# Kernel optimization log

Measured on AMD Instinct MI355X. Metric: run time of the kernel, lower is better.

## Reference

```python
import jax, jax.numpy as jnp
import numpy as np
from math import sqrt

B, LT, LM = 4, 512, 1024
HID, NH, HD = 512, 8, 64          # self-attn: hidden, n_head, head_size
NHP, KS = 16, 64                  # cross-attn: 2*max_charge*n_head_per_mass, key_size
FF = 4 * HID
ALPHA = 2.0
EPS = 1e-5


def apply_rope(x, dis):
    # dis: same trailing dim as x; chunk into (sin, cos) halves
    s, c = jnp.split(dis, 2, axis=-1)
    x0, x1 = x[..., 0::2], x[..., 1::2]
    return jnp.concatenate([x0 * c - x1 * s, x1 * c + x0 * s], axis=-1)


def layer_norm(x, g, b):
    mu = jnp.mean(x, axis=-1, keepdims=True)
    var = jnp.mean(jnp.square(x - mu), axis=-1, keepdims=True)
    return (x - mu) * jax.lax.rsqrt(var + EPS) * g + b


def deep_norm(x, postx, g, b):
    # dropout is identity in eval mode
    return layer_norm(x * ALPHA + postx, g, b)


def attn_block(x_q, x_kv, dis_q, dis_k, wq, bq, wk, bk, wv, bv, wo, bo, mask, n_head, head_size):
    bsz = x_q.shape[0]
    q = (x_q @ wq.T + bq).reshape(bsz, -1, n_head, head_size)
    k = (x_kv @ wk.T + bk).reshape(bsz, -1, n_head, head_size)
    v = (x_kv @ wv.T + bv).reshape(bsz, -1, n_head, head_size)
    q = apply_rope(q, dis_q)
    k = apply_rope(k, dis_k)
    attn = jnp.einsum('bnhd,bmhd->bhnm', q, k) / sqrt(head_size)  # [B,H,Lq,Lk]
    attn = jnp.where(mask, attn, -jnp.inf)
    attn = jax.nn.softmax(attn, axis=-1)
    out = jnp.einsum('bhnm,bmhd->bnhd', attn, v).reshape(bsz, -1, n_head * head_size)
    return out @ wo.T + bo


def setup_inputs() -> dict:
    key = jax.random.key(0)
    ks = jax.random.split(key, 32)
    rn = lambda i, shape, s=1.0: jax.random.normal(ks[i], shape, jnp.float32) * s
    inp = {}
    inp['tgt'] = rn(0, (B, LT, HID))
    inp['mem'] = rn(1, (B, LM, HID))
    inp['glycan_mass'] = rn(2, (B, LT, NH, HD))
    inp['glycan_query_mass'] = rn(3, (B, LT, NH, HD))
    inp['glycan_crossattn_mass'] = rn(4, (B, LT, NHP, KS))
    inp['node_mass_emb'] = rn(5, (B, LM, NHP, KS))
    inp['node_mass'] = rn(6, (B, LM))
    causal = jnp.tril(jnp.ones((LT, LT), bool))
    inp['tgt_mask'] = jnp.broadcast_to(causal[None, None], (B, 1, LT, LT))
    inp['rel_mask'] = jnp.ones((B, 1, LT, LM), bool)
    inp['layer'] = 0
    inp['A'] = rn(7, (1,))
    w = 0.03  # param init scale
    # self-attn params
    inp['wq1'] = rn(8, (HID, HID), w);  inp['bq1'] = jnp.zeros((HID,))
    inp['wk1'] = rn(9, (HID, HID), w);  inp['bk1'] = jnp.zeros((HID,))
    inp['wv1'] = rn(10, (HID, HID), w); inp['bv1'] = jnp.zeros((HID,))
    inp['wo1'] = rn(11, (HID, HID), w); inp['bo1'] = jnp.zeros((HID,))
    inp['ln1_g'] = jnp.ones((HID,));    inp['ln1_b'] = jnp.zeros((HID,))
    # cross-attn params (projection dim NHP*KS = 1024)
    P = NHP * KS
    inp['wq2'] = rn(12, (P, HID), w);   inp['bq2'] = jnp.zeros((P,))
    inp['wk2'] = rn(13, (P, HID), w);   inp['bk2'] = jnp.zeros((P,))
    inp['wv2'] = rn(14, (P, HID), w);   inp['bv2'] = jnp.zeros((P,))
    inp['wo2'] = rn(15, (HID, P), w);   inp['bo2'] = jnp.zeros((HID,))
    inp['ln2_g'] = jnp.ones((HID,));    inp['ln2_b'] = jnp.zeros((HID,))
    # FFN params (no bias) + DeepNorm LN
    inp['w_ff1'] = rn(16, (FF, HID), w)
    inp['w_ff2'] = rn(17, (HID, FF), w)
    inp['ln3_g'] = jnp.ones((HID,));    inp['ln3_b'] = jnp.zeros((HID,))
    return inp


def reference(tgt, mem, glycan_mass, glycan_query_mass, glycan_crossattn_mass,
              node_mass_emb, node_mass, tgt_mask, rel_mask, layer, A,
              wq1, bq1, wk1, bk1, wv1, bv1, wo1, bo1, ln1_g, ln1_b,
              wq2, bq2, wk2, bk2, wv2, bv2, wo2, bo2, ln2_g, ln2_b,
              w_ff1, w_ff2, ln3_g, ln3_b):
    # masked self-attention with mass RoPE + DeepNorm
    postx = attn_block(tgt, tgt, glycan_query_mass, glycan_mass,
                       wq1, bq1, wk1, bk1, wv1, bv1, wo1, bo1,
                       tgt_mask, NH, HD)
    tgt = deep_norm(tgt, postx, ln1_g, ln1_b)
    # cross-attention with mass RoPE + DeepNorm (node_mass, layer, A unused in math)
    postx = attn_block(tgt, mem, glycan_crossattn_mass, node_mass_emb,
                       wq2, bq2, wk2, bk2, wv2, bv2, wo2, bo2,
                       rel_mask, NHP, KS)
    tgt = deep_norm(tgt, postx, ln2_g, ln2_b)
    # FFN + DeepNorm
    postx = jax.nn.relu(tgt @ w_ff1.T) @ w_ff2.T
    tgt = deep_norm(tgt, postx, ln3_g, ln3_b)
    return (tgt, A)
```

## Files before the change

kernel.cpp:

```cpp
#include <hip/hip_runtime.h>
#include <hip/hip_bf16.h>
#include <math.h>

#define EPS 1e-5f

typedef __attribute__((ext_vector_type(8))) __bf16 bf16x8;
typedef __attribute__((ext_vector_type(4))) float f32x4;

struct CvtJobs {
    const float* src[12];
    __bf16* dst[12];
    int off[13];
};

__global__ __launch_bounds__(256) void cvt_k(CvtJobs J, int total) {
    int g = blockIdx.x * 256 + threadIdx.x;
    if (g >= total) return;
    int j = 0;
    #pragma unroll
    for (int t = 0; t < 11; ++t) j += (g >= J.off[t + 1]) ? 1 : 0;
    int lg = g - J.off[j];
    const float* s = J.src[j] + (size_t)lg * 8;
    float4 a = *(const float4*)s;
    float4 b = *(const float4*)(s + 4);
    bf16x8 o;
    o[0] = (__bf16)a.x; o[1] = (__bf16)a.y; o[2] = (__bf16)a.z; o[3] = (__bf16)a.w;
    o[4] = (__bf16)b.x; o[5] = (__bf16)b.y; o[6] = (__bf16)b.z; o[7] = (__bf16)b.w;
    *(bf16x8*)(J.dst[j] + (size_t)lg * 8) = o;
}

template<int BT, int KS, typename OutT, bool RELU, bool HAS_BIAS, bool ROPE>
__global__ __launch_bounds__(256) void gemm_bf16_k(const __bf16* __restrict__ A,
                                                   const __bf16* __restrict__ W,
                                                   const float* __restrict__ b0,
                                                   const float* __restrict__ b1,
                                                   const float* __restrict__ b2,
                                                   int bshift,
                                                   const float* __restrict__ disK,
                                                   int ropeLo, int ropeHi, int dstride,
                                                   OutT* __restrict__ C,
                                                   int M, int N, int K) {
    constexpr int NI = BT / 32;
    __shared__ __bf16 As[BT * 64];
    __shared__ __bf16 Ws[BT * 64];

    const int tid  = threadIdx.x;
    const int wave = tid >> 6;
    const int lane = tid & 63;
    const int frow = lane & 15;
    const int fgrp = lane >> 4;

    const int nb  = gridDim.x * gridDim.y;
    const int bid = blockIdx.y * gridDim.x + blockIdx.x;
    const int v   = (bid & 7) * (nb >> 3) + (bid >> 3);
    const int bx  = (v % gridDim.x) * BT;
    const int by  = (v / gridDim.x) * BT;

    const int Kc = K / KS;
    const int kbeg = blockIdx.z * Kc;
    OutT* Cz = C + (size_t)blockIdx.z * M * N;

    const int wr = (wave >> 1) * (BT / 2);
    const int wc = (wave & 1) * (BT / 2);
    const int ldr = lane >> 3;
    const int ldc = (lane & 7) * 8;

    f32x4 acc[NI][NI] = {};

    for (int k0 = kbeg; k0 < kbeg + Kc; k0 += 64) {
        #pragma unroll
        for (int it = 0; it < NI; ++it) {
            int chunk = it * 4 + wave;
            int r = chunk * 8 + ldr;
            const __bf16* ga = A + (size_t)(by + r) * K + k0 + ldc;
            const __bf16* gw = W + (size_t)(bx + r) * K + k0 + ldc;
            __builtin_amdgcn_global_load_lds(
                (const __attribute__((address_space(1))) unsigned int*)ga,
                (__attribute__((address_space(3))) unsigned int*)(As + chunk * 512),
                16, 0, 0);
            __builtin_amdgcn_global_load_lds(
                (const __attribute__((address_space(1))) unsigned int*)gw,
                (__attribute__((address_space(3))) unsigned int*)(Ws + chunk * 512),
                16, 0, 0);
        }
        __syncthreads();

        #pragma unroll
        for (int kk = 0; kk < 2; ++kk) {
            bf16x8 af[NI], wf[NI];
            #pragma unroll
            for (int i = 0; i < NI; ++i)
                af[i] = *(const bf16x8*)&As[(wr + i * 16 + frow) * 64 + kk * 32 + fgrp * 8];
            #pragma unroll
            for (int j = 0; j < NI; ++j)
                wf[j] = *(const bf16x8*)&Ws[(wc + j * 16 + frow) * 64 + kk * 32 + fgrp * 8];
            #pragma unroll
            for (int i = 0; i < NI; ++i)
                #pragma unroll
                for (int j = 0; j < NI; ++j)
                    acc[i][j] = __builtin_amdgcn_mfma_f32_16x16x32_bf16(af[i], wf[j], acc[i][j], 0, 0, 0);
        }
        __syncthreads();
    }

    #pragma unroll
    for (int i = 0; i < NI; ++i) {
        #pragma unroll
        for (int jj = 0; jj < 4; ++jj) {
            int row = by + wr + i * 16 + fgrp * 4 + jj;
            #pragma unroll
            for (int j = 0; j < NI; ++j) {
                int col = bx + wc + j * 16 + frow;
                float val = acc[i][j][jj];
                if (HAS_BIAS) {
                    int sel = col >> bshift;
                    const float* bp = sel == 0 ? b0 : (sel == 1 ? b1 : b2);
                    val += bp[col & (int)((1u << bshift) - 1)];
                }
                if (RELU) val = fmaxf(val, 0.0f);
                if (ROPE && col >= ropeLo && col < ropeHi) {
                    int hcol = col & 63;
                    int p = hcol >> 1;
                    int hbase = col - hcol;
                    const float* dr = disK + (size_t)row * dstride + (hbase - ropeLo);
                    float sv = dr[p], cv = dr[32 + p];
                    float pv = __shfl_xor(val, 1);
                    val = ((col & 1) == 0) ? (val * cv - pv * sv)
                                           : (val * cv + pv * sv);
                }
                Cz[(size_t)row * N + col] = (OutT)val;
            }
        }
    }
}

template<int KS>
__global__ __launch_bounds__(256) void gemm_wo_k(const __bf16* __restrict__ Opart,
                                                 const float* __restrict__ lsums,
                                                 int prows, int H,
                                                 const __bf16* __restrict__ W,
                                                 float* __restrict__ C,
                                                 int M, int N, int K) {
    __shared__ __bf16 As[64 * 64];
    __shared__ __bf16 Ws[64 * 64];

    const int tid  = threadIdx.x;
    const int wave = tid >> 6;
    const int lane = tid & 63;
    const int frow = lane & 15;
    const int fgrp = lane >> 4;

    const int nb  = gridDim.x * gridDim.y;
    const int bid = blockIdx.y * gridDim.x + blockIdx.x;
    const int v   = (bid & 7) * (nb >> 3) + (bid >> 3);
    const int bx  = (v % gridDim.x) * 64;
    const int by  = (v / gridDim.x) * 64;

    const int Kc = K / KS;
    const int kbeg = blockIdx.z * Kc;
    float* Cz = C + (size_t)blockIdx.z * M * N;

    const int wr = (wave >> 1) * 32;
    const int wc = (wave & 1) * 32;
    const int ldr = lane >> 3;
    const int ldc = (lane & 7) * 8;

    f32x4 acc[2][2] = {};

    for (int k0 = kbeg; k0 < kbeg + Kc; k0 += 64) {
        const int h = k0 >> 6;
        #pragma unroll
        for (int it = 0; it < 2; ++it) {
            int chunk = it * 4 + wave;
            int r = chunk * 8 + ldr;
            size_t rid = (size_t)(by + r) * H + h;
            bf16x8 o0 = *(const bf16x8*)&Opart[rid * 64 + ldc];
            bf16x8 o1 = *(const bf16x8*)&Opart[((size_t)prows + rid) * 64 + ldc];
            float li = 1.0f / (lsums[rid] + lsums[prows + rid]);
            bf16x8 m;
            #pragma unroll
            for (int u = 0; u < 8; ++u)
                m[u] = (__bf16)(((float)o0[u] + (float)o1[u]) * li);
            *(bf16x8*)&As[chunk * 512 + lane * 8] = m;
            const __bf16* gw = W + (size_t)(bx + r) * K + k0 + ldc;
            __builtin_amdgcn_global_load_lds(
                (const __attribute__((address_space(1))) unsigned int*)gw,
                (__attribute__((address_space(3))) unsigned int*)(Ws + chunk * 512),
                16, 0, 0);
        }
        __syncthreads();

        #pragma unroll
        for (int kk = 0; kk < 2; ++kk) {
            bf16x8 af[2], wf[2];
            #pragma unroll
            for (int i = 0; i < 2; ++i)
                af[i] = *(const bf16x8*)&As[(wr + i * 16 + frow) * 64 + kk * 32 + fgrp * 8];
            #pragma unroll
            for (int j = 0; j < 2; ++j)
                wf[j] = *(const bf16x8*)&Ws[(wc + j * 16 + frow) * 64 + kk * 32 + fgrp * 8];
            #pragma unroll
            for (int i = 0; i < 2; ++i)
                #pragma unroll
                for (int j = 0; j < 2; ++j)
                    acc[i][j] = __builtin_amdgcn_mfma_f32_16x16x32_bf16(af[i], wf[j], acc[i][j], 0, 0, 0);
        }
        __syncthreads();
    }

    #pragma unroll
    for (int i = 0; i < 2; ++i)
        #pragma unroll
        for (int jj = 0; jj < 4; ++jj) {
            int row = by + wr + i * 16 + fgrp * 4 + jj;
            #pragma unroll
            for (int j = 0; j < 2; ++j) {
                int col = bx + wc + j * 16 + frow;
                Cz[(size_t)row * N + col] = acc[i][j][jj];
            }
        }
}

template<bool CAUSAL, int NSPLIT>
__global__ __launch_bounds__(256) void attn_bf16_k(const __bf16* __restrict__ Q,
                                                   const __bf16* __restrict__ K,
                                                   const __bf16* __restrict__ V,
                                                   const float* __restrict__ disQ,
                                                   __bf16* __restrict__ Opart,
                                                   float* __restrict__ lsums,
                                                   int H, int LQ, int LM,
                                                   int qstride, int kvstride,
                                                   int prows) {
    __shared__ __bf16 Ks[64 * 72];
    __shared__ __bf16 Vt[64 * 72];
    __shared__ __bf16 Ps[4 * 16 * 72];

    const int nqt = LQ >> 6;
    const int nb  = gridDim.x;
    const int bid = blockIdx.x;
    const int v   = (bid & 7) * (nb >> 3) + (bid >> 3);
    int t = v;
    const int qt = t % nqt; t /= nqt;
    const int chunk = t % NSPLIT; t /= NSPLIT;
    const int h = t % H;
    const int b = t / H;
    const int q0 = qt * 64;

    const int tid  = threadIdx.x;
    const int wave = tid >> 6;
    const int lane = tid & 63;
    const int frow = lane & 15;
    const int fgrp = lane >> 4;

    const int qrow = q0 + wave * 16 + frow;
    bf16x8 qf0, qf1;
    {
        const __bf16* qp = Q + ((size_t)b * LQ + qrow) * qstride + h * 64 + fgrp * 8;
        bf16x8 xa = *(const bf16x8*)qp;
        bf16x8 xb = *(const bf16x8*)(qp + 32);
        const float* dq = disQ + (((size_t)b * LQ + qrow) * H + h) * 64;
        #pragma unroll
        for (int u = 0; u < 4; ++u) {
            float sv = dq[fgrp * 4 + u], cv = dq[32 + fgrp * 4 + u];
            float x0 = (float)xa[2 * u], x1 = (float)xa[2 * u + 1];
            qf0[2 * u]     = (__bf16)(x0 * cv - x1 * sv);
            qf0[2 * u + 1] = (__bf16)(x1 * cv + x0 * sv);
            sv = dq[16 + fgrp * 4 + u]; cv = dq[48 + fgrp * 4 + u];
            x0 = (float)xb[2 * u]; x1 = (float)xb[2 * u + 1];
            qf1[2 * u]     = (__bf16)(x0 * cv - x1 * sv);
            qf1[2 * u + 1] = (__bf16)(x1 * cv + x0 * sv);
        }
    }

    f32x4 oacc[4] = {};
    float lsum[4] = {};

    const int kbAll = CAUSAL ? (qt + 1) : (LM >> 6);
    const int kcnt  = (LM >> 6) / NSPLIT;
    const int kb0   = chunk * kcnt;
    const int kb1   = min(kbAll, kb0 + kcnt);

    const int r   = tid >> 2;
    const int c0q = tid & 3;
    const int kphys = (r & 7) + 8 * ((r >> 3) ^ (2 * c0q));

    for (int kb = kb0; kb < kb1; ++kb) {
        const int m0 = kb * 64;
        {
            const __bf16* kp = K + ((size_t)b * LM + m0 + r) * kvstride + h * 64 + c0q * 16;
            *(bf16x8*)&Ks[r * 72 + c0q * 16]     = *(const bf16x8*)kp;
            *(bf16x8*)&Ks[r * 72 + c0q * 16 + 8] = *(const bf16x8*)(kp + 8);
        }
        {
            const __bf16* vp = V + ((size_t)b * LM + m0 + r) * kvstride + h * 64 + c0q * 16;
            bf16x8 va = *(const bf16x8*)vp;
            bf16x8 vb = *(const bf16x8*)(vp + 8);
            #pragma unroll
            for (int j = 0; j < 8; ++j) {
                Vt[(c0q * 16 + j) * 72 + kphys]     = va[j];
                Vt[(c0q * 16 + 8 + j) * 72 + kphys] = vb[j];
            }
        }
        __syncthreads();

        f32x4 s[4];
        #pragma unroll
        for (int n = 0; n < 4; ++n) {
            bf16x8 kf0 = *(const bf16x8*)&Ks[(n * 16 + frow) * 72 + fgrp * 8];
            bf16x8 kf1 = *(const bf16x8*)&Ks[(n * 16 + frow) * 72 + 32 + fgrp * 8];
            f32x4 tt = {0.f, 0.f, 0.f, 0.f};
            tt = __builtin_amdgcn_mfma_f32_16x16x32_bf16(qf0, kf0, tt, 0, 0, 0);
            tt = __builtin_amdgcn_mfma_f32_16x16x32_bf16(qf1, kf1, tt, 0, 0, 0);
            s[n] = tt;
        }

        #pragma unroll
        for (int n = 0; n < 4; ++n)
            #pragma unroll
            for (int jj = 0; jj < 4; ++jj) {
                bool valid = (!CAUSAL) ||
                    ((m0 + n * 16 + frow) <= (q0 + wave * 16 + fgrp * 4 + jj));
                s[n][jj] = valid ? __expf(s[n][jj] * 0.125f - 8.0f) : 0.0f;
            }

        #pragma unroll
        for (int jj = 0; jj < 4; ++jj) {
            float rs = (s[0][jj] + s[1][jj]) + (s[2][jj] + s[3][jj]);
            #pragma unroll
            for (int msk = 8; msk >= 1; msk >>= 1) rs += __shfl_xor(rs, msk);
            lsum[jj] += rs;
        }

        #pragma unroll
        for (int n = 0; n < 4; ++n)
            #pragma unroll
            for (int jj = 0; jj < 4; ++jj) {
                int q = fgrp * 4 + jj;
                int kidx = (frow & 7) + 8 * (((2 * n) + (frow >> 3)) ^ (2 * ((q >> 3) & 1)));
                Ps[wave * 1152 + q * 72 + kidx] = (__bf16)s[n][jj];
            }

        #pragma unroll
        for (int c = 0; c < 2; ++c) {
            int pblk = (c * 4 + fgrp) ^ (2 * ((frow >> 3) & 1));
            bf16x8 pf = *(const bf16x8*)&Ps[wave * 1152 + frow * 72 + 8 * pblk];
            #pragma unroll
            for (int n = 0; n < 4; ++n) {
                int vblk = (c * 4 + fgrp) ^ (2 * n);
                bf16x8 vf = *(const bf16x8*)&Vt[(n * 16 + frow) * 72 + 8 * vblk];
                oacc[n] = __builtin_amdgcn_mfma_f32_16x16x32_bf16(pf, vf, oacc[n], 0, 0, 0);
            }
        }
        __syncthreads();
    }

    #pragma unroll
    for (int jj = 0; jj < 4; ++jj) {
        int q = q0 + wave * 16 + fgrp * 4 + jj;
        size_t ridx = (size_t)chunk * prows + ((size_t)b * LQ + q) * H + h;
        if (frow == 0) lsums[ridx] = lsum[jj];
        #pragma unroll
        for (int n = 0; n < 4; ++n)
            Opart[ridx * 64 + n * 16 + frow] = (__bf16)oacc[n][jj];
    }
}

template<int NP, bool HASB, bool WRITE_BF>
__global__ __launch_bounds__(256) void deepnorm_k(const float* __restrict__ x,
                                                  const float* __restrict__ p0,
                                                  const float* __restrict__ p1,
                                                  const float* __restrict__ p2,
                                                  const float* __restrict__ p3,
                                                  const float* __restrict__ bias,
                                                  const float* __restrict__ g,
                                                  const float* __restrict__ b,
                                                  float* __restrict__ out,
                                                  __bf16* __restrict__ out_bf,
                                                  const float* __restrict__ Ain,
                                                  float* __restrict__ Aout) {
    int row = blockIdx.x;
    int tid = threadIdx.x;
    if (Aout && row == 0 && tid == 0) Aout[0] = Ain[0];
    size_t i0 = (size_t)row * 512 + tid, i1 = i0 + 256;
    float a0 = p0[i0], a1 = p0[i1];
    if (NP > 1) { a0 += p1[i0]; a1 += p1[i1]; }
    if (NP > 2) { a0 += p2[i0]; a1 += p2[i1]; }
    if (NP > 3) { a0 += p3[i0]; a1 += p3[i1]; }
    if (HASB)   { a0 += bias[tid]; a1 += bias[tid + 256]; }
    float v0 = x[i0] * 2.0f + a0;
    float v1 = x[i1] * 2.0f + a1;

    __shared__ float red[4];
    int wave = tid >> 6, lane = tid & 63;

    float s = v0 + v1;
    #pragma unroll
    for (int o = 32; o >= 1; o >>= 1) s += __shfl_xor(s, o);
    if (lane == 0) red[wave] = s;
    __syncthreads();
    float mean = (red[0] + red[1] + red[2] + red[3]) * (1.0f / 512.0f);

    float d0 = v0 - mean, d1 = v1 - mean;
    float vs = d0 * d0 + d1 * d1;
    #pragma unroll
    for (int o = 32; o >= 1; o >>= 1) vs += __shfl_xor(vs, o);
    __syncthreads();
    if (lane == 0) red[wave] = vs;
    __syncthreads();
    float var = (red[0] + red[1] + red[2] + red[3]) * (1.0f / 512.0f);
    float inv = rsqrtf(var + EPS);

    float o0 = d0 * inv * g[tid] + b[tid];
    float o1 = d1 * inv * g[tid + 256] + b[tid + 256];
    out[i0] = o0;
    out[i1] = o1;
    if (WRITE_BF) {
        out_bf[i0] = (__bf16)o0;
        out_bf[i1] = (__bf16)o1;
    }
}

extern "C" void kernel_launch(void* const* d_in, const int* in_sizes, int n_in,
                              void* d_out, int out_size, void* d_ws, size_t ws_size,
                              hipStream_t stream) {
    const float* tgt  = (const float*)d_in[0];
    const float* mem  = (const float*)d_in[1];
    const float* dis_k1 = (const float*)d_in[2];
    const float* dis_q1 = (const float*)d_in[3];
    const float* dis_q2 = (const float*)d_in[4];
    const float* dis_k2 = (const float*)d_in[5];
    const float* A_in   = (const float*)d_in[10];
    const float* wq1 = (const float*)d_in[11]; const float* bq1 = (const float*)d_in[12];
    const float* wk1 = (const float*)d_in[13]; const float* bk1 = (const float*)d_in[14];
    const float* wv1 = (const float*)d_in[15]; const float* bv1 = (const float*)d_in[16];
    const float* wo1 = (const float*)d_in[17]; const float* bo1 = (const float*)d_in[18];
    const float* ln1g = (const float*)d_in[19]; const float* ln1b = (const float*)d_in[20];
    const float* wq2 = (const float*)d_in[21]; const float* bq2 = (const float*)d_in[22];
    const float* wk2 = (const float*)d_in[23]; const float* bk2 = (const float*)d_in[24];
    const float* wv2 = (const float*)d_in[25]; const float* bv2 = (const float*)d_in[26];
    const float* wo2 = (const float*)d_in[27]; const float* bo2 = (const float*)d_in[28];
    const float* ln2g = (const float*)d_in[29]; const float* ln2b = (const float*)d_in[30];
    const float* wff1 = (const float*)d_in[31]; const float* wff2 = (const float*)d_in[32];
    const float* ln3g = (const float*)d_in[33]; const float* ln3b = (const float*)d_in[34];

    char* ws = (char*)d_ws;
    auto MB = [&](size_t mb) { return ws + mb * 1024 * 1024; };

    __bf16* wqkv1_bf = (__bf16*)MB(0);
    __bf16* wo1_bf   = (__bf16*)MB(2);
    __bf16* wq2_bf   = (__bf16*)MB(3);
    __bf16* wkv2_bf  = (__bf16*)MB(4);
    __bf16* wo2_bf   = (__bf16*)MB(6);
    __bf16* wff1_bf  = (__bf16*)MB(7);
    __bf16* wff2_bf  = (__bf16*)MB(9);
    __bf16* tgt_bf   = (__bf16*)MB(11);
    __bf16* mem_bf   = (__bf16*)MB(13);
    __bf16* qkv1_bf  = (__bf16*)MB(17);
    __bf16* Opart    = (__bf16*)MB(25);
    float*  x1       = (float*)MB(41);
    float*  post0    = (float*)MB(45);
    float*  post1    = (float*)MB(49);
    float*  post2    = (float*)MB(53);
    float*  post3    = (float*)MB(57);
    __bf16* kv2_bf   = (__bf16*)MB(45);
    float*  x2       = (float*)MB(65);
    __bf16* x2_bf    = (__bf16*)MB(69);
    float*  lsums    = (float*)MB(71);
    __bf16* x1_bf    = tgt_bf;
    __bf16* q2_bf    = qkv1_bf;
    __bf16* ffh_bf   = Opart;

    float* out = (float*)d_out;

    CvtJobs J;
    const float* srcs[12] = {tgt, mem, wq1, wk1, wv1, wo1, wq2, wk2, wv2, wo2, wff1, wff2};
    __bf16* dsts[12] = {tgt_bf, mem_bf, wqkv1_bf, wqkv1_bf + 262144, wqkv1_bf + 524288,
                        wo1_bf, wq2_bf, wkv2_bf, wkv2_bf + 524288, wo2_bf, wff1_bf, wff2_bf};
    int sizes[12] = {2048 * 512, 4096 * 512, 512 * 512, 512 * 512, 512 * 512, 512 * 512,
                     1024 * 512, 1024 * 512, 1024 * 512, 1024 * 512, 2048 * 512, 512 * 2048};
    int acc = 0;
    for (int i = 0; i < 12; ++i) { J.src[i] = srcs[i]; J.dst[i] = dsts[i]; J.off[i] = acc; acc += sizes[i] / 8; }
    J.off[12] = acc;
    cvt_k<<<(acc + 255) / 256, 256, 0, stream>>>(J, acc);

    gemm_bf16_k<64, 1, __bf16, false, true, true><<<dim3(24, 32), 256, 0, stream>>>(
        tgt_bf, wqkv1_bf, bq1, bk1, bv1, 9, dis_k1, 512, 1024, 512,
        qkv1_bf, 2048, 1536, 512);
    attn_bf16_k<true, 2><<<512, 256, 0, stream>>>(qkv1_bf, qkv1_bf + 512, qkv1_bf + 1024,
                                                  dis_q1, Opart, lsums,
                                                  8, 512, 512, 1536, 1536, 16384);
    gemm_wo_k<2><<<dim3(8, 32, 2), 256, 0, stream>>>(Opart, lsums, 16384, 8,
                                                     wo1_bf, post0, 2048, 512, 512);
    deepnorm_k<2, true, true><<<2048, 256, 0, stream>>>(tgt, post0, post1, nullptr, nullptr,
                                                        bo1, ln1g, ln1b, x1, x1_bf,
                                                        nullptr, nullptr);

    gemm_bf16_k<64, 1, __bf16, false, true, false><<<dim3(16, 32), 256, 0, stream>>>(
        x1_bf, wq2_bf, bq2, bq2, bq2, 31, nullptr, 0, 0, 0,
        q2_bf, 2048, 1024, 512);
    gemm_bf16_k<64, 1, __bf16, false, true, true><<<dim3(32, 64), 256, 0, stream>>>(
        mem_bf, wkv2_bf, bk2, bv2, bv2, 10, dis_k2, 0, 1024, 1024,
        kv2_bf, 4096, 2048, 512);
    attn_bf16_k<false, 2><<<1024, 256, 0, stream>>>(q2_bf, kv2_bf, kv2_bf + 1024,
                                                    dis_q2, Opart, lsums,
                                                    16, 512, 1024, 1024, 2048, 32768);
    gemm_wo_k<2><<<dim3(8, 32, 2), 256, 0, stream>>>(Opart, lsums, 32768, 16,
                                                     wo2_bf, post0, 2048, 512, 1024);
    deepnorm_k<2, true, true><<<2048, 256, 0, stream>>>(x1, post0, post1, nullptr, nullptr,
                                                        bo2, ln2g, ln2b, x2, x2_bf,
                                                        nullptr, nullptr);

    gemm_bf16_k<64, 1, __bf16, true, false, false><<<dim3(32, 32), 256, 0, stream>>>(
        x2_bf, wff1_bf, nullptr, nullptr, nullptr, 31, nullptr, 0, 0, 0,
        ffh_bf, 2048, 2048, 512);
    gemm_bf16_k<64, 4, float, false, false, false><<<dim3(8, 32, 4), 256, 0, stream>>>(
        ffh_bf, wff2_bf, nullptr, nullptr, nullptr, 31, nullptr, 0, 0, 0,
        post0, 2048, 512, 2048);
    deepnorm_k<4, false, false><<<2048, 256, 0, stream>>>(x2, post0, post1, post2, post3,
                                                          nullptr, ln3g, ln3b, out, nullptr,
                                                          A_in, out + 2048 * 512);
}
```

Measured before the change: 176.5 us.

## Fuse fp32-to-bf16 conversion into GEMM loads and double attention KV splits

Drops the standalone conversion kernel: GEMMs now read fp32 weights (and fp32 activations for tgt/mem) and convert to bf16 while staging into shared memory, with multi-source weight selection for the concatenated QKV/KV projections. The attention kernels use 4 KV splits instead of 2, and the output-projection kernel reduces over NS partials. MFMA sections get s_setprio hints. This removes one launch and a full read/write pass over the converted tensors. In exchange, converted weights are re-read in fp32 by every block tile, and register-staged loads replace the async global-to-LDS path, which may cost bandwidth and latency.

```diff
diff --git a/kernel.cpp b/kernel.cpp
--- a/kernel.cpp
+++ b/kernel.cpp
@@ -7,39 +7,29 @@
 typedef __attribute__((ext_vector_type(8))) __bf16 bf16x8;
 typedef __attribute__((ext_vector_type(4))) float f32x4;
 
-struct CvtJobs {
-    const float* src[12];
-    __bf16* dst[12];
-    int off[13];
-};
-
-__global__ __launch_bounds__(256) void cvt_k(CvtJobs J, int total) {
-    int g = blockIdx.x * 256 + threadIdx.x;
-    if (g >= total) return;
-    int j = 0;
-    #pragma unroll
-    for (int t = 0; t < 11; ++t) j += (g >= J.off[t + 1]) ? 1 : 0;
-    int lg = g - J.off[j];
-    const float* s = J.src[j] + (size_t)lg * 8;
-    float4 a = *(const float4*)s;
-    float4 b = *(const float4*)(s + 4);
+__device__ __forceinline__ bf16x8 cvt8(const float* p) {
+    float4 a = *(const float4*)p;
+    float4 b = *(const float4*)(p + 4);
     bf16x8 o;
     o[0] = (__bf16)a.x; o[1] = (__bf16)a.y; o[2] = (__bf16)a.z; o[3] = (__bf16)a.w;
     o[4] = (__bf16)b.x; o[5] = (__bf16)b.y; o[6] = (__bf16)b.z; o[7] = (__bf16)b.w;
-    *(bf16x8*)(J.dst[j] + (size_t)lg * 8) = o;
+    return o;
 }
 
-template<int BT, int KS, typename OutT, bool RELU, bool HAS_BIAS, bool ROPE>
-__global__ __launch_bounds__(256) void gemm_bf16_k(const __bf16* __restrict__ A,
-                                                   const __bf16* __restrict__ W,
-                                                   const float* __restrict__ b0,
-                                                   const float* __restrict__ b1,
-                                                   const float* __restrict__ b2,
-                                                   int bshift,
-                                                   const float* __restrict__ disK,
-                                                   int ropeLo, int ropeHi, int dstride,
-                                                   OutT* __restrict__ C,
-                                                   int M, int N, int K) {
+template<int BT, int KS, typename OutT, bool RELU, bool HAS_BIAS, bool ROPE, bool AF32>
+__global__ __launch_bounds__(256) void gemm_k(const void* __restrict__ Av,
+                                              const float* __restrict__ W0,
+                                              const float* __restrict__ W1,
+                                              const float* __restrict__ W2,
+                                              int wshift,
+                                              const float* __restrict__ b0,
+                                              const float* __restrict__ b1,
+                                              const float* __restrict__ b2,
+                                              int bshift,
+                                              const float* __restrict__ disK,
+                                              int ropeLo, int ropeHi, int dstride,
+                                              OutT* __restrict__ C,
+                                              int M, int N, int K) {
     constexpr int NI = BT / 32;
     __shared__ __bf16 As[BT * 64];
     __shared__ __bf16 Ws[BT * 64];
@@ -65,6 +55,8 @@
     const int ldr = lane >> 3;
     const int ldc = (lane & 7) * 8;
 
+    const unsigned wmask = (wshift >= 31) ? 0x7FFFFFFFu : ((1u << wshift) - 1);
+
     f32x4 acc[NI][NI] = {};
 
     for (int k0 = kbeg; k0 < kbeg + Kc; k0 += 64) {
@@ -72,16 +64,23 @@
         for (int it = 0; it < NI; ++it) {
             int chunk = it * 4 + wave;
             int r = chunk * 8 + ldr;
-            const __bf16* ga = A + (size_t)(by + r) * K + k0 + ldc;
-            const __bf16* gw = W + (size_t)(bx + r) * K + k0 + ldc;
-            __builtin_amdgcn_global_load_lds(
-                (const __attribute__((address_space(1))) unsigned int*)ga,
-                (__attribute__((address_space(3))) unsigned int*)(As + chunk * 512),
-                16, 0, 0);
-            __builtin_amdgcn_global_load_lds(
-                (const __attribute__((address_space(1))) unsigned int*)gw,
-                (__attribute__((address_space(3))) unsigned int*)(Ws + chunk * 512),
-                16, 0, 0);
+            if constexpr (AF32) {
+                const float* ga = (const float*)Av + (size_t)(by + r) * K + k0 + ldc;
+                *(bf16x8*)&As[chunk * 512 + lane * 8] = cvt8(ga);
+            } else {
+                const __bf16* ga = (const __bf16*)Av + (size_t)(by + r) * K + k0 + ldc;
+                __builtin_amdgcn_global_load_lds(
+                    (const __attribute__((address_space(1))) unsigned int*)ga,
+                    (__attribute__((address_space(3))) unsigned int*)(As + chunk * 512),
+                    16, 0, 0);
+            }
+            {
+                int wrow = bx + r;
+                int sel = wrow >> wshift;
+                const float* wp = sel == 0 ? W0 : (sel == 1 ? W1 : W2);
+                const float* gw = wp + (size_t)(wrow & wmask) * K + k0 + ldc;
+                *(bf16x8*)&Ws[chunk * 512 + lane * 8] = cvt8(gw);
+            }
         }
         __syncthreads();
 
@@ -115,7 +114,7 @@
                 if (HAS_BIAS) {
                     int sel = col >> bshift;
                     const float* bp = sel == 0 ? b0 : (sel == 1 ? b1 : b2);
-                    val += bp[col & (int)((1u << bshift) - 1)];
+                    val += bp[col & (int)((bshift >= 31) ? 0x7FFFFFFFu : ((1u << bshift) - 1))];
                 }
                 if (RELU) val = fmaxf(val, 0.0f);
                 if (ROPE && col >= ropeLo && col < ropeHi) {
@@ -134,11 +133,11 @@
     }
 }
 
-template<int KS>
+template<int NS, int KS>
 __global__ __launch_bounds__(256) void gemm_wo_k(const __bf16* __restrict__ Opart,
                                                  const float* __restrict__ lsums,
                                                  int prows, int H,
-                                                 const __bf16* __restrict__ W,
+                                                 const float* __restrict__ W,
                                                  float* __restrict__ C,
                                                  int M, int N, int K) {
     __shared__ __bf16 As[64 * 64];
@@ -174,19 +173,28 @@
             int chunk = it * 4 + wave;
             int r = chunk * 8 + ldr;
             size_t rid = (size_t)(by + r) * H + h;
-            bf16x8 o0 = *(const bf16x8*)&Opart[rid * 64 + ldc];
-            bf16x8 o1 = *(const bf16x8*)&Opart[((size_t)prows + rid) * 64 + ldc];
-            float li = 1.0f / (lsums[rid] + lsums[prows + rid]);
+            float o[8] = {};
+            float den = 0.f;
+            #pragma unroll
+            for (int i = 0; i < NS; ++i) {
+                size_t base = ((size_t)i * prows + rid);
+                bf16x8 ov = *(const bf16x8*)&Opart[base * 64 + ldc];
+                den += lsums[base];
+                #pragma unroll
+                for (int u = 0; u < 8; ++u) o[u] += (float)ov[u];
+            }
+            float li = 1.0f / den;
             bf16x8 m;
             #pragma unroll
-            for (int u = 0; u < 8; ++u)
-                m[u] = (__bf16)(((float)o0[u] + (float)o1[u]) * li);
+            for (int u = 0; u < 8; ++u) m[u] = (__bf16)(o[u] * li);
             *(bf16x8*)&As[chunk * 512 + lane * 8] = m;
-            const __bf16* gw = W + (size_t)(bx + r) * K + k0 + ldc;
-            __builtin_amdgcn_global_load_lds(
-                (const __attribute__((address_space(1))) unsigned int*)gw,
-                (__attribute__((address_space(3))) unsigned int*)(Ws + chunk * 512),
-                16, 0, 0);
+            const float* gw = W + (size_t)(bx + r) * K + k0 + ldc;
+            float4 fa = *(const float4*)gw;
+            float4 fb = *(const float4*)(gw + 4);
+            bf16x8 wv;
+            wv[0] = (__bf16)fa.x; wv[1] = (__bf16)fa.y; wv[2] = (__bf16)fa.z; wv[3] = (__bf16)fa.w;
+            wv[4] = (__bf16)fb.x; wv[5] = (__bf16)fb.y; wv[6] = (__bf16)fb.z; wv[7] = (__bf16)fb.w;
+            *(bf16x8*)&Ws[chunk * 512 + lane * 8] = wv;
         }
         __syncthreads();
 
@@ -304,6 +312,7 @@
         __syncthreads();
 
         f32x4 s[4];
+        __builtin_amdgcn_s_setprio(1);
         #pragma unroll
         for (int n = 0; n < 4; ++n) {
             bf16x8 kf0 = *(const bf16x8*)&Ks[(n * 16 + frow) * 72 + fgrp * 8];
@@ -313,6 +322,7 @@
             tt = __builtin_amdgcn_mfma_f32_16x16x32_bf16(qf1, kf1, tt, 0, 0, 0);
             s[n] = tt;
         }
+        __builtin_amdgcn_s_setprio(0);
 
         #pragma unroll
         for (int n = 0; n < 4; ++n)
@@ -340,6 +350,7 @@
                 Ps[wave * 1152 + q * 72 + kidx] = (__bf16)s[n][jj];
             }
 
+        __builtin_amdgcn_s_setprio(1);
         #pragma unroll
         for (int c = 0; c < 2; ++c) {
             int pblk = (c * 4 + fgrp) ^ (2 * ((frow >> 3) & 1));
@@ -351,6 +362,7 @@
                 oacc[n] = __builtin_amdgcn_mfma_f32_16x16x32_bf16(pf, vf, oacc[n], 0, 0, 0);
             }
         }
+        __builtin_amdgcn_s_setprio(0);
         __syncthreads();
     }
 
@@ -446,75 +458,55 @@
     char* ws = (char*)d_ws;
     auto MB = [&](size_t mb) { return ws + mb * 1024 * 1024; };
 
-    __bf16* wqkv1_bf = (__bf16*)MB(0);
-    __bf16* wo1_bf   = (__bf16*)MB(2);
-    __bf16* wq2_bf   = (__bf16*)MB(3);
-    __bf16* wkv2_bf  = (__bf16*)MB(4);
-    __bf16* wo2_bf   = (__bf16*)MB(6);
-    __bf16* wff1_bf  = (__bf16*)MB(7);
-    __bf16* wff2_bf  = (__bf16*)MB(9);
-    __bf16* tgt_bf   = (__bf16*)MB(11);
-    __bf16* mem_bf   = (__bf16*)MB(13);
-    __bf16* qkv1_bf  = (__bf16*)MB(17);
-    __bf16* Opart    = (__bf16*)MB(25);
-    float*  x1       = (float*)MB(41);
-    float*  post0    = (float*)MB(45);
-    float*  post1    = (float*)MB(49);
-    float*  post2    = (float*)MB(53);
-    float*  post3    = (float*)MB(57);
-    __bf16* kv2_bf   = (__bf16*)MB(45);
-    float*  x2       = (float*)MB(65);
-    __bf16* x2_bf    = (__bf16*)MB(69);
-    float*  lsums    = (float*)MB(71);
-    __bf16* x1_bf    = tgt_bf;
+    __bf16* qkv1_bf  = (__bf16*)MB(0);
+    __bf16* Opart    = (__bf16*)MB(8);
+    float*  x1       = (float*)MB(24);
+    float*  post0    = (float*)MB(28);
+    float*  post1    = (float*)MB(32);
+    float*  post2    = (float*)MB(36);
+    float*  post3    = (float*)MB(40);
+    __bf16* kv2_bf   = (__bf16*)MB(28);
+    float*  x2       = (float*)MB(44);
+    __bf16* x2_bf    = (__bf16*)MB(48);
+    float*  lsums    = (float*)MB(50);
+    __bf16* x1_bf    = (__bf16*)MB(51);
     __bf16* q2_bf    = qkv1_bf;
     __bf16* ffh_bf   = Opart;
 
     float* out = (float*)d_out;
 
-    CvtJobs J;
-    const float* srcs[12] = {tgt, mem, wq1, wk1, wv1, wo1, wq2, wk2, wv2, wo2, wff1, wff2};
-    __bf16* dsts[12] = {tgt_bf, mem_bf, wqkv1_bf, wqkv1_bf + 262144, wqkv1_bf + 524288,
-                        wo1_bf, wq2_bf, wkv2_bf, wkv2_bf + 524288, wo2_bf, wff1_bf, wff2_bf};
-    int sizes[12] = {2048 * 512, 4096 * 512, 512 * 512, 512 * 512, 512 * 512, 512 * 512,
-                     1024 * 512, 1024 * 512, 1024 * 512, 1024 * 512, 2048 * 512, 512 * 2048};
-    int acc = 0;
-    for (int i = 0; i < 12; ++i) { J.src[i] = srcs[i]; J.dst[i] = dsts[i]; J.off[i] = acc; acc += sizes[i] / 8; }
-    J.off[12] = acc;
-    cvt_k<<<(acc + 255) / 256, 256, 0, stream>>>(J, acc);
-
-    gemm_bf16_k<64, 1, __bf16, false, true, true><<<dim3(24, 32), 256, 0, stream>>>(
-        tgt_bf, wqkv1_bf, bq1, bk1, bv1, 9, dis_k1, 512, 1024, 512,
+    gemm_k<64, 1, __bf16, false, true, true, true><<<dim3(24, 32), 256, 0, stream>>>(
+        tgt, wq1, wk1, wv1, 9, bq1, bk1, bv1, 9, dis_k1, 512, 1024, 512,
         qkv1_bf, 2048, 1536, 512);
-    attn_bf16_k<true, 2><<<512, 256, 0, stream>>>(qkv1_bf, qkv1_bf + 512, qkv1_bf + 1024,
-                                                  dis_q1, Opart, lsums,
-                                                  8, 512, 512, 1536, 1536, 16384);
-    gemm_wo_k<2><<<dim3(8, 32, 2), 256, 0, stream>>>(Opart, lsums, 16384, 8,
-                                                     wo1_bf, post0, 2048, 512, 512);
+    attn_bf16_k<true, 4><<<1024, 256, 0, stream>>>(qkv1_bf, qkv1_bf + 512, qkv1_bf + 1024,
+                                                   dis_q1, Opart, lsums,
+                                                   8, 512, 512, 1536, 1536, 16384);
+    gemm_wo_k<4, 2><<<dim3(8, 32, 2), 256, 0, stream>>>(Opart, lsums, 16384, 8,
+                                                        wo1, post0, 2048, 512, 512);
     deepnorm_k<2, true, true><<<2048, 256, 0, stream>>>(tgt, post0, post1, nullptr, nullptr,
                                                         bo1, ln1g, ln1b, x1, x1_bf,
                                                         nullptr, nullptr);
 
-    gemm_bf16_k<64, 1, __bf16, false, true, false><<<dim3(16, 32), 256, 0, stream>>>(
-        x1_bf, wq2_bf, bq2, bq2, bq2, 31, nullptr, 0, 0, 0,
+    gemm_k<64, 1, __bf16, false, true, false, false><<<dim3(16, 32), 256, 0, stream>>>(
+        x1_bf, wq2, wq2, wq2, 31, bq2, bq2, bq2, 31, nullptr, 0, 0, 0,
         q2_bf, 2048, 1024, 512);
-    gemm_bf16_k<64, 1, __bf16, false, true, true><<<dim3(32, 64), 256, 0, stream>>>(
-        mem_bf, wkv2_bf, bk2, bv2, bv2, 10, dis_k2, 0, 1024, 1024,
+    gemm_k<64, 1, __bf16, false, true, true, true><<<dim3(32, 64), 256, 0, stream>>>(
+        mem, wk2, wv2, wv2, 10, bk2, bv2, bv2, 10, dis_k2, 0, 1024, 1024,
         kv2_bf, 4096, 2048, 512);
-    attn_bf16_k<false, 2><<<1024, 256, 0, stream>>>(q2_bf, kv2_bf, kv2_bf + 1024,
+    attn_bf16_k<false, 4><<<2048, 256, 0, stream>>>(q2_bf, kv2_bf, kv2_bf + 1024,
                                                     dis_q2, Opart, lsums,
                                                     16, 512, 1024, 1024, 2048, 32768);
-    gemm_wo_k<2><<<dim3(8, 32, 2), 256, 0, stream>>>(Opart, lsums, 32768, 16,
-                                                     wo2_bf, post0, 2048, 512, 1024);
+    gemm_wo_k<4, 2><<<dim3(8, 32, 2), 256, 0, stream>>>(Opart, lsums, 32768, 16,
+                                                        wo2, post0, 2048, 512, 1024);
     deepnorm_k<2, true, true><<<2048, 256, 0, stream>>>(x1, post0, post1, nullptr, nullptr,
                                                         bo2, ln2g, ln2b, x2, x2_bf,
                                                         nullptr, nullptr);
 
-    gemm_bf16_k<64, 1, __bf16, true, false, false><<<dim3(32, 32), 256, 0, stream>>>(
-        x2_bf, wff1_bf, nullptr, nullptr, nullptr, 31, nullptr, 0, 0, 0,
+    gemm_k<64, 1, __bf16, true, false, false, false><<<dim3(32, 32), 256, 0, stream>>>(
+        x2_bf, wff1, wff1, wff1, 31, nullptr, nullptr, nullptr, 31, nullptr, 0, 0, 0,
         ffh_bf, 2048, 2048, 512);
-    gemm_bf16_k<64, 4, float, false, false, false><<<dim3(8, 32, 4), 256, 0, stream>>>(
-        ffh_bf, wff2_bf, nullptr, nullptr, nullptr, 31, nullptr, 0, 0, 0,
+    gemm_k<64, 4, float, false, false, false, false><<<dim3(8, 32, 4), 256, 0, stream>>>(
+        ffh_bf, wff2, wff2, wff2, 31, nullptr, nullptr, nullptr, 31, nullptr, 0, 0, 0,
         post0, 2048, 512, 2048);
     deepnorm_k<4, false, false><<<2048, 256, 0, stream>>>(x2, post0, post1, post2, post3,
                                                           nullptr, ln3g, ln3b, out, nullptr,
```

Result: slower. 195.4 us (+10.7%).
